# Optimization experiments

Measured on AMD Instinct MI355X. Metric: run time of the kernel, lower is better.

## Reference

```python
import jax, jax.numpy as jnp
import numpy as np

B, SM, SI, D, H, FF = 4, 1024, 4096, 256, 8, 1024
EPS = 1e-6

def _ln(x, g, b):
    m = jnp.mean(x, axis=-1, keepdims=True)
    v = jnp.mean(jnp.square(x - m), axis=-1, keepdims=True)
    return (x - m) * jax.lax.rsqrt(v + EPS) * g + b

def setup_inputs() -> dict:
    key = jax.random.key(0)
    ks = jax.random.split(key, 12)
    s = 0.02
    return {
        "state_seq": jax.random.normal(ks[0], (B, SM, D), jnp.float32),
        "input_seq": jax.random.normal(ks[1], (B, SI, D), jnp.float32),
        "Wk": jax.random.normal(ks[2], (D, D), jnp.float32) * s,
        "bk": jnp.zeros((D,), jnp.float32),
        "Wv": jax.random.normal(ks[3], (D, D), jnp.float32) * s,
        "bv": jnp.zeros((D,), jnp.float32),
        "Wq": jax.random.normal(ks[4], (H, D, D), jnp.float32) * s,
        "bq": jnp.zeros((H, D), jnp.float32),
        "Wo": jax.random.normal(ks[5], (H * D, D), jnp.float32) * s,
        "bo": jnp.zeros((D,), jnp.float32),
        "ln1_g": jnp.ones((D,), jnp.float32),
        "ln1_b": jnp.zeros((D,), jnp.float32),
        "W_in": jax.random.normal(ks[6], (D, FF), jnp.float32) * s,
        "b_in": jnp.zeros((FF,), jnp.float32),
        "Wg_nl": jax.random.normal(ks[7], (FF, FF), jnp.float32) * s,
        "bg_nl": jnp.zeros((FF,), jnp.float32),
        "Wg_l": jax.random.normal(ks[8], (FF, FF), jnp.float32) * s,
        "bg_l": jnp.zeros((FF,), jnp.float32),
        "Wg_o": jax.random.normal(ks[9], (FF, D), jnp.float32) * s,
        "bg_o": jnp.zeros((D,), jnp.float32),
        "ln2_g": jnp.ones((D,), jnp.float32),
        "ln2_b": jnp.zeros((D,), jnp.float32),
    }

def reference(state_seq, input_seq, Wk, bk, Wv, bv, Wq, bq, Wo, bo,
              ln1_g, ln1_b, W_in, b_in, Wg_nl, bg_nl, Wg_l, bg_l, Wg_o, bg_o,
              ln2_g, ln2_b):
    # shared key/value projections (multi-query: one K/V, many Q)
    ik = input_seq @ Wk + bk            # [B,SI,D]
    mk = state_seq @ Wk + bk            # [B,SM,D]
    iv = input_seq @ Wv + bv            # [B,SI,D]
    mv = state_seq @ Wv + bv            # [B,SM,D]
    # per-head queries from memory cells, stacked over H
    q = jnp.einsum('bmd,hde->hbme', state_seq, Wq) + bq[:, None, None, :]  # [H,B,SM,D]
    input_score = jnp.einsum('hbme,bse->hbms', q, ik)                      # [H,B,SM,SI]
    self_score = jnp.sum(q * mk[None], axis=-1, keepdims=True)             # [H,B,SM,1]
    score = jnp.concatenate([self_score, input_score], axis=-1)
    score = score / jnp.sqrt(jnp.asarray(D, score.dtype))
    attn = jax.nn.softmax(score, axis=-1)                                  # [H,B,SM,1+SI]
    val = jnp.einsum('hbms,bse->hbme', attn[..., 1:], iv) + attn[..., 0:1] * mv[None]
    concat = jnp.transpose(val, (1, 2, 0, 3)).reshape(val.shape[1], val.shape[2], -1)  # [B,SM,H*D]
    attn_out = concat @ Wo + bo
    x = _ln(attn_out + state_seq, ln1_g, ln1_b)
    h = jax.nn.relu(x @ W_in + b_in)                                       # [B,SM,FF]
    g = jax.nn.relu(h @ Wg_nl + bg_nl) * (h @ Wg_l + bg_l)
    ff = g @ Wg_o + bg_o
    return _ln(ff + x, ln2_g, ln2_b)
```

## Files before the change

### kernel.cpp

```cpp
#include <hip/hip_runtime.h>
#include <hip/hip_bf16.h>

typedef __bf16 bfx8 __attribute__((ext_vector_type(8)));
typedef __bf16 bfx4 __attribute__((ext_vector_type(4)));
typedef float  f32x4 __attribute__((ext_vector_type(4)));
typedef float  f32x16 __attribute__((ext_vector_type(16)));

#define MFMA16(a,b,c) __builtin_amdgcn_mfma_f32_16x16x32_bf16((a),(b),(c),0,0,0)
#define MFMA32(a,b,c) __builtin_amdgcn_mfma_f32_32x32x16_bf16((a),(b),(c),0,0,0)


#define PSCALE 0.09016844f
#define PCLAMP 43.2808512f

__device__ __forceinline__ unsigned cvtpk_bf16(float lo, float hi) {
  unsigned d;
  asm("v_cvt_pk_bf16_f32 %0, %1, %2" : "=v"(d) : "v"(lo), "v"(hi));
  return d;
}

__device__ __forceinline__ bfx8 packswap(const float* p) {
  unsigned a = cvtpk_bf16(p[0], p[1]);
  unsigned b = cvtpk_bf16(p[2], p[3]);
  unsigned c = cvtpk_bf16(p[4], p[5]);
  unsigned d = cvtpk_bf16(p[6], p[7]);
  asm("v_permlane32_swap_b32 %0, %1" : "+v"(a), "+v"(c));
  asm("v_permlane32_swap_b32 %0, %1" : "+v"(b), "+v"(d));
  union { unsigned u[4]; bfx8 v; } uu;
  uu.u[0] = a; uu.u[1] = b; uu.u[2] = c; uu.u[3] = d;
  return uu.v;
}

__device__ __forceinline__ void tile_tr(const float* __restrict__ src, __bf16* __restrict__ dst,
                                        int R, int C, int tile, float (*lt)[65]) {
  int tpr = C >> 6;
  int tr = tile / tpr, tc = tile % tpr;
  int c  = threadIdx.x & 63;
  int r0 = (threadIdx.x >> 6) << 4;
  const float* sp = src + (long)(tr * 64 + r0) * C + tc * 64 + c;
#pragma unroll
  for (int i = 0; i < 16; i++) lt[r0 + i][c] = sp[(long)i * C];
  __syncthreads();
  __bf16* dp = dst + (long)(tc * 64 + r0) * R + tr * 64 + c;
#pragma unroll
  for (int i = 0; i < 16; i++) dp[(long)i * R] = (__bf16)lt[c][r0 + i];
}

__global__ void trans_attn_t(const float* __restrict__ Wk, const float* __restrict__ Wv,
                             const float* __restrict__ Wq, const float* __restrict__ Wo,
                             __bf16* __restrict__ wkvqt, __bf16* __restrict__ wot) {
  __shared__ float lt[64][65];
  int t = blockIdx.x;
  if (t < 16)       tile_tr(Wk, wkvqt, 256, 256, t, lt);
  else if (t < 32)  tile_tr(Wv, wkvqt + 65536, 256, 256, t - 16, lt);
  else if (t < 160) {
    int e = t - 32, m = e >> 4;
    tile_tr(Wq + (long)m * 65536, wkvqt + 131072 + (long)m * 65536, 256, 256, e & 15, lt);
  } else            tile_tr(Wo, wot, 2048, 256, t - 160, lt);
}

__global__ void trans_ffn_t(const float* __restrict__ W_in, const float* __restrict__ Wg_nl,
                            const float* __restrict__ Wg_l, const float* __restrict__ Wg_o,
                            __bf16* __restrict__ dst) {
  __shared__ float lt[64][65];
  int t = blockIdx.x;
  if (t < 64)       tile_tr(W_in, dst, 256, 1024, t, lt);
  else if (t < 320) tile_tr(Wg_nl, dst + 262144, 1024, 1024, t - 64, lt);
  else if (t < 576) tile_tr(Wg_l, dst + 1310720, 1024, 1024, t - 320, lt);
  else              tile_tr(Wg_o, dst + 2359296, 1024, 256, t - 576, lt);
}

__device__ __forceinline__
void gemm_body(const __bf16* __restrict__ Xb, const float* __restrict__ Xf,
               const __bf16* __restrict__ Wt,
               const float* __restrict__ b1, const float* __restrict__ b2,
               const float* __restrict__ b3,
               __bf16* __restrict__ C, __bf16* __restrict__ C2, __bf16* __restrict__ C3,
               float* __restrict__ Cf,
               int M, int N, int Kfull, int kspan, int xmode, int mode, int act,
               int bx, int by, int bz, __bf16* xs, __bf16* wsm) {
  const int tid  = threadIdx.x;
  const int lane = tid & 63;
  const int w    = tid >> 6;
  const int l15  = lane & 15;
  const int quad = lane >> 4;
  const int wm   = (w >> 1) * 64;
  const int wn   = (w & 1) * 64;
  const int m0   = bx * 128;
  const int n0   = by * 128;
  const int k0   = (mode == 7) ? bz * kspan : 0;

  f32x4 acc[4][4];
#pragma unroll
  for (int i = 0; i < 4; i++)
#pragma unroll
    for (int j = 0; j < 4; j++) acc[i][j] = (f32x4){0.f, 0.f, 0.f, 0.f};

  for (int kk = k0; kk < k0 + kspan; kk += 64) {
    __syncthreads();
#pragma unroll
    for (int rep = 0; rep < 4; rep++) {
      int idx = rep * 256 + tid;
      int row = idx >> 3;
      int g   = idx & 7;
      if (xmode == 1) {
        const float* p = Xf + (long)(m0 + row) * Kfull + kk + g * 8;
        f32x4 a0 = *(const f32x4*)p;
        f32x4 a1 = *(const f32x4*)(p + 4);
        bfx8 v;
#pragma unroll
        for (int j = 0; j < 4; j++) { v[j] = (__bf16)a0[j]; v[4 + j] = (__bf16)a1[j]; }
        *(bfx8*)&xs[row * 72 + g * 8] = v;
      } else if (xmode == 2) {
        const __bf16* p = Xb + (long)(m0 + row) * 2048 + kk + g * 8;
        bfx8 a = *(const bfx8*)p;
        bfx8 bb = *(const bfx8*)(p + 1024);
        bfx8 v;
#pragma unroll
        for (int j = 0; j < 8; j++) v[j] = (__bf16)((float)a[j] * (float)bb[j]);
        *(bfx8*)&xs[row * 72 + g * 8] = v;
      } else {
        *(bfx8*)&xs[row * 72 + g * 8] = *(const bfx8*)(Xb + (long)(m0 + row) * Kfull + kk + g * 8);
      }
      *(bfx8*)&wsm[row * 72 + g * 8] = *(const bfx8*)(Wt + (long)(n0 + row) * Kfull + kk + g * 8);
    }
    __syncthreads();
#pragma unroll
    for (int ks = 0; ks < 2; ks++) {
      bfx8 af[4], bf_[4];
#pragma unroll
      for (int i = 0; i < 4; i++) af[i]  = *(const bfx8*)&xs[(wm + 16 * i + l15) * 72 + ks * 32 + quad * 8];
#pragma unroll
      for (int j = 0; j < 4; j++) bf_[j] = *(const bfx8*)&wsm[(wn + 16 * j + l15) * 72 + ks * 32 + quad * 8];
#pragma unroll
      for (int i = 0; i < 4; i++)
#pragma unroll
        for (int j = 0; j < 4; j++) acc[i][j] = MFMA16(af[i], bf_[j], acc[i][j]);
    }
  }

#pragma unroll
  for (int j = 0; j < 4; j++) {
    int n = n0 + wn + 16 * j + l15;
    float bv;
    if (mode == 4)      bv = (n < 256) ? b1[n] : b2[n - 256];
    else if (mode == 5) bv = (n < 256) ? b1[n] : (n < 512) ? b2[n - 256] : b3[n - 512];
    else if (mode == 6) bv = (n < 1024) ? b1[n] : b2[n - 1024];
    else if (mode == 7) bv = (bz == 0) ? b1[n] : 0.f;
    else                bv = b1[n];
#pragma unroll
    for (int i = 0; i < 4; i++) {
#pragma unroll
      for (int r = 0; r < 4; r++) {
        int m = m0 + wm + 16 * i + quad * 4 + r;
        float v = acc[i][j][r] + bv;
        if (mode == 6) { if (n < 1024) v = fmaxf(v, 0.f); }
        else if (act == 1) v = fmaxf(v, 0.f);
        if (mode == 4) {
          if (n < 256) C[(long)m * 256 + n] = (__bf16)v;
          else {
            int bb_ = m >> 12, si = m & 4095;
            C2[((long)(bb_ * 128 + (si >> 5)) * 256 + (n - 256)) * 32 + (si & 31)] = (__bf16)v;
          }
        } else if (mode == 5) {
          if (n < 256)      C[(long)m * 256 + n] = (__bf16)v;
          else if (n < 512) C2[(long)m * 256 + (n - 256)] = (__bf16)v;
          else {
            int nn = n - 512, hhh = nn >> 8, dd = nn & 255;
            C3[(long)hhh * 1048576 + (long)m * 256 + dd] = (__bf16)v;
          }
        } else if (mode == 7) {
          Cf[(long)bz * M * N + (long)m * N + n] = v;
        } else {
          C[(long)m * N + n] = (__bf16)v;
        }
      }
    }
  }
}

__global__ __launch_bounds__(256)
void gemm_bt(const __bf16* Xb, const float* Xf, const __bf16* Wt,
             const float* b1, const float* b2, const float* b3,
             __bf16* C, __bf16* C2, __bf16* C3, float* Cf,
             int M, int N, int Kfull, int kspan, int xmode, int mode, int act) {
  __shared__ __bf16 xs[128 * 72];
  __shared__ __bf16 wsm[128 * 72];
  gemm_body(Xb, Xf, Wt, b1, b2, b3, C, C2, C3, Cf, M, N, Kfull, kspan, xmode, mode, act,
            blockIdx.x, blockIdx.y, blockIdx.z, xs, wsm);
}

__global__ __launch_bounds__(256)
void proj2(const float* input, const float* state, const __bf16* Wkvqt,
           const float* bk, const float* bv, const float* bq,
           __bf16* ik, __bf16* ivT, __bf16* mk, __bf16* mv, __bf16* qbuf) {
  __shared__ __bf16 xs[128 * 72];
  __shared__ __bf16 wsm[128 * 72];
  int bid = blockIdx.x;
  if (bid < 512) {
    gemm_body(nullptr, input, Wkvqt, bk, bv, nullptr, ik, ivT, nullptr, nullptr,
              16384, 512, 256, 256, 1, 4, 0, bid & 127, bid >> 7, 0, xs, wsm);
  } else {
    int b2 = bid - 512;
    gemm_body(nullptr, state, Wkvqt, bk, bv, bq, mk, mv, qbuf, nullptr,
              4096, 2560, 256, 256, 1, 5, 0, b2 & 31, b2 >> 5, 0, xs, wsm);
  }
}

__global__ __attribute__((amdgpu_flat_work_group_size(512, 512)))
__attribute__((amdgpu_waves_per_eu(2, 2)))
void attn_kernel(const __bf16* __restrict__ qb,
                 const __bf16* __restrict__ ik,
                 const __bf16* __restrict__ ivT,
                 const __bf16* __restrict__ mk,
                 const __bf16* __restrict__ mv,
                 __bf16* __restrict__ concat) {
  __shared__ union {
    struct {
      __bf16 lk[2][2][32][264];
      __bf16 lvt[2][2][256][40];
    } s;
    float ex[4 * 8192 + 128];
  } sm;

  const int tid  = threadIdx.x;
  const int lane = tid & 63;
  const int w    = tid >> 6;
  const int half = w >> 2;
  const int wq   = w & 3;
  const int t256 = tid & 255;
  const int l31  = lane & 31;
  const int h    = lane >> 5;

  const int m0 = blockIdx.x * 128;
  const int b  = blockIdx.y;
  const int hh = blockIdx.z;
  const int mw = m0 + wq * 32;
  const int c0 = half * 64;

  const long qbase  = ((long)hh * 4096 + b * 1024 + mw) * 256;
  const long kvbase = (long)b * 4096 * 256;
  const long vtbase = (long)b * 128 * 8192;
  const long mbase  = ((long)b * 1024 + mw) * 256;

  bfx8 qf[16];
  {
    const __bf16* qrow = qb + qbase + (long)l31 * 256 + h * 8;
#pragma unroll
    for (int kt = 0; kt < 16; kt++) qf[kt] = *(const bfx8*)(qrow + kt * 16);
  }

  float ps_l;
  {
    const __bf16* krow = mk + mbase + (long)l31 * 256 + h * 8;
    float s = 0.f;
#pragma unroll
    for (int kt = 0; kt < 16; kt++) {
      bfx8 kv = *(const bfx8*)(krow + kt * 16);
#pragma unroll
      for (int j = 0; j < 8; j++) s += (float)qf[kt][j] * (float)kv[j];
    }
    s += __shfl_xor(s, 32);
    ps_l = __builtin_amdgcn_exp2f(fminf(s * PSCALE, PCLAMP));
  }

  f32x16 oacc[8];
#pragma unroll
  for (int dt = 0; dt < 8; dt++)
#pragma unroll
    for (int i = 0; i < 16; i++) oacc[dt][i] = 0.f;
  float den_l = 0.f;
  bfx8 pf0c, pf1c;

  f32x16 zz;
#pragma unroll
  for (int i = 0; i < 16; i++) zz[i] = 0.f;

  auto sload_k = [&](int c, bfx8* kreg) {
    const long kb = kvbase + (long)c * 8192;
#pragma unroll
    for (int rep = 0; rep < 4; rep++) {
      int idx = rep * 256 + t256;
      kreg[rep] = *(const bfx8*)(ik + kb + (long)(idx >> 5) * 256 + (idx & 31) * 8);
    }
  };
  auto sload_v = [&](int c, bfx8* vreg) {
    const long vb = vtbase + (long)c * 8192;
#pragma unroll
    for (int rep = 0; rep < 4; rep++) {
      int idx = rep * 256 + t256;
      vreg[rep] = *(const bfx8*)(ivT + vb + (long)idx * 8);
    }
  };
  auto sstore_k = [&](int slot, const bfx8* kreg) {
#pragma unroll
    for (int rep = 0; rep < 4; rep++) {
      int idx = rep * 256 + t256;
      *(bfx8*)&sm.s.lk[half][slot][idx >> 5][(idx & 31) * 8] = kreg[rep];
    }
  };
  auto sstore_v = [&](int slot, const bfx8* vreg) {
#pragma unroll
    for (int rep = 0; rep < 4; rep++) {
      int idx = rep * 256 + t256;
      *(bfx8*)&sm.s.lvt[half][slot][idx >> 2][(idx & 3) * 8] = vreg[rep];
    }
  };

  auto chunkMFMA = [&](int vslot, int kslot, bool doS, bool doPV, f32x16* sa) {
#pragma unroll
    for (int t = 0; t < 8; t++) {
      bfx8 vf0, vf1, kf0, kf1;
      if (doPV) {
        vf0 = *(const bfx8*)&sm.s.lvt[half][vslot][t * 32 + l31][h * 8];
        vf1 = *(const bfx8*)&sm.s.lvt[half][vslot][t * 32 + l31][16 + h * 8];
      }
      if (doS) {
        kf0 = *(const bfx8*)&sm.s.lk[half][kslot][l31][(2 * t) * 16 + h * 8];
        kf1 = *(const bfx8*)&sm.s.lk[half][kslot][l31][(2 * t + 1) * 16 + h * 8];
      }
      if (doPV) oacc[t] = MFMA32(pf0c, vf0, oacc[t]);
      if (doS) {
        if (t < 2) sa[2 * t] = MFMA32(kf0, qf[2 * t], zz);
        else       sa[(2 * t) & 3] = MFMA32(kf0, qf[2 * t], sa[(2 * t) & 3]);
      }
      if (doPV) oacc[t] = MFMA32(pf1c, vf1, oacc[t]);
      if (doS) {
        if (t < 2) sa[2 * t + 1] = MFMA32(kf1, qf[2 * t + 1], zz);
        else       sa[(2 * t + 1) & 3] = MFMA32(kf1, qf[2 * t + 1], sa[(2 * t + 1) & 3]);
      }
    }
  };

  auto finishP = [&](const f32x16* sa) {
    float p[16];
#pragma unroll
    for (int r = 0; r < 16; r++) {
      float s = (sa[0][r] + sa[1][r]) + (sa[2][r] + sa[3][r]);
      p[r] = __builtin_amdgcn_exp2f(fminf(s * PSCALE, PCLAMP));
      den_l += p[r];
    }
    pf0c = packswap(p);
    pf1c = packswap(p + 8);
  };

  {
    bfx8 kreg[4], vreg[4];
    sload_k(c0, kreg);
    sload_v(c0, vreg);
    sstore_k(0, kreg);
    sstore_v(0, vreg);
    sload_k(c0 + 1, kreg);
    sstore_k(1, kreg);
  }
  __syncthreads();

  f32x16 sa[4];
  chunkMFMA(0, 0, true, false, sa);
  finishP(sa);
  __syncthreads();

  for (int i = 0; i < 62; i++) {
    bfx8 kreg[4], vreg[4];
    sload_k(c0 + i + 2, kreg);
    sload_v(c0 + i + 1, vreg);
    chunkMFMA(i & 1, (i + 1) & 1, true, true, sa);
    sstore_k(i & 1, kreg);
    sstore_v((i + 1) & 1, vreg);
    finishP(sa);
    __syncthreads();
  }
  {
    bfx8 vreg[4];
    sload_v(c0 + 63, vreg);
    chunkMFMA(0, 1, true, true, sa);
    sstore_v(1, vreg);
    finishP(sa);
    __syncthreads();
  }
  chunkMFMA(1, 0, false, true, sa);
  __syncthreads();

  float den_row = den_l + __shfl_xor(den_l, 32);
  if (half == 1) {
    float* eo = sm.ex + wq * 8192;
#pragma unroll
    for (int dt = 0; dt < 8; dt++)
#pragma unroll
      for (int rq = 0; rq < 4; rq++) {
        f32x4 v4 = { oacc[dt][rq * 4 + 0], oacc[dt][rq * 4 + 1],
                     oacc[dt][rq * 4 + 2], oacc[dt][rq * 4 + 3] };
        *(f32x4*)&eo[(dt * 4 + rq) * 256 + lane * 4] = v4;
      }
    if (h == 0) sm.ex[4 * 8192 + wq * 32 + l31] = den_row;
  }
  __syncthreads();
  if (half == 0) {
    const float* eo = sm.ex + wq * 8192;
#pragma unroll
    for (int dt = 0; dt < 8; dt++)
#pragma unroll
      for (int rq = 0; rq < 4; rq++) {
        f32x4 v4 = *(const f32x4*)&eo[(dt * 4 + rq) * 256 + lane * 4];
#pragma unroll
        for (int j = 0; j < 4; j++) oacc[dt][rq * 4 + j] += v4[j];
      }
    float den1 = sm.ex[4 * 8192 + wq * 32 + l31];
    float tot  = den_row + den1 + ps_l;

#pragma unroll
    for (int r = 0; r < 16; r++) {
      int row = (r & 3) + 8 * (r >> 2) + 4 * h;
      float ps   = __shfl(ps_l, row);
      float dinv = 1.f / __shfl(tot, row);
      const __bf16* mvrow = mv + mbase + (long)row * 256;
      __bf16* crow = concat + ((long)(b * 1024 + mw + row)) * 2048 + hh * 256;
#pragma unroll
      for (int dt = 0; dt < 8; dt++) {
        int d = dt * 32 + l31;
        crow[d] = (__bf16)((oacc[dt][r] + ps * (float)mvrow[d]) * dinv);
      }
    }
  }
}

__global__ __launch_bounds__(256)
void attn_kernel_f(const __bf16* __restrict__ qb, const __bf16* __restrict__ ik,
                   const __bf16* __restrict__ ivT, const __bf16* __restrict__ mk,
                   const __bf16* __restrict__ mv, __bf16* __restrict__ concat) {
  __shared__ __bf16 lk[2][32][264];
  __shared__ __bf16 lvt[2][256][40];

  const int tid  = threadIdx.x;
  const int lane = tid & 63;
  const int w    = tid >> 6;
  const int l31  = lane & 31;
  const int h    = lane >> 5;

  const int m0 = blockIdx.x * 128;
  const int b  = blockIdx.y;
  const int hh = blockIdx.z;
  const int mw = m0 + w * 32;

  const long qbase  = ((long)hh * 4096 + b * 1024 + mw) * 256;
  const long kvbase = (long)b * 4096 * 256;
  const long vtbase = (long)b * 128 * 8192;
  const long mbase  = ((long)b * 1024 + mw) * 256;

  bfx8 qf[16];
  {
    const __bf16* qrow = qb + qbase + (long)l31 * 256 + h * 8;
#pragma unroll
    for (int kt = 0; kt < 16; kt++) qf[kt] = *(const bfx8*)(qrow + kt * 16);
  }

  float ps_l;
  {
    const __bf16* krow = mk + mbase + (long)l31 * 256 + h * 8;
    float s = 0.f;
#pragma unroll
    for (int kt = 0; kt < 16; kt++) {
      bfx8 kv = *(const bfx8*)(krow + kt * 16);
#pragma unroll
      for (int j = 0; j < 8; j++) s += (float)qf[kt][j] * (float)kv[j];
    }
    s += __shfl_xor(s, 32);
    ps_l = __builtin_amdgcn_exp2f(fminf(s * PSCALE, PCLAMP));
  }

  f32x16 oacc[8];
#pragma unroll
  for (int dt = 0; dt < 8; dt++)
#pragma unroll
    for (int i = 0; i < 16; i++) oacc[dt][i] = 0.f;
  float den_l = 0.f;
  bfx8 pf0c, pf1c;

  f32x16 zz;
#pragma unroll
  for (int i = 0; i < 16; i++) zz[i] = 0.f;

  auto sload_k = [&](int c, bfx8* kreg) {
    const long kb = kvbase + (long)c * 8192;
#pragma unroll
    for (int rep = 0; rep < 4; rep++) {
      int idx = rep * 256 + tid;
      kreg[rep] = *(const bfx8*)(ik + kb + (long)(idx >> 5) * 256 + (idx & 31) * 8);
    }
  };
  auto sload_v = [&](int c, bfx8* vreg) {
    const long vb = vtbase + (long)c * 8192;
#pragma unroll
    for (int rep = 0; rep < 4; rep++) {
      int idx = rep * 256 + tid;
      vreg[rep] = *(const bfx8*)(ivT + vb + (long)idx * 8);
    }
  };
  auto sstore_k = [&](int slot, const bfx8* kreg) {
#pragma unroll
    for (int rep = 0; rep < 4; rep++) {
      int idx = rep * 256 + tid;
      *(bfx8*)&lk[slot][idx >> 5][(idx & 31) * 8] = kreg[rep];
    }
  };
  auto sstore_v = [&](int slot, const bfx8* vreg) {
#pragma unroll
    for (int rep = 0; rep < 4; rep++) {
      int idx = rep * 256 + tid;
      *(bfx8*)&lvt[slot][idx >> 2][(idx & 3) * 8] = vreg[rep];
    }
  };

  auto chunkMFMA = [&](int vslot, int kslot, bool doS, bool doPV, f32x16* sa) {
#pragma unroll
    for (int t = 0; t < 8; t++) {
      bfx8 vf0, vf1, kf0, kf1;
      if (doPV) {
        vf0 = *(const bfx8*)&lvt[vslot][t * 32 + l31][h * 8];
        vf1 = *(const bfx8*)&lvt[vslot][t * 32 + l31][16 + h * 8];
      }
      if (doS) {
        kf0 = *(const bfx8*)&lk[kslot][l31][(2 * t) * 16 + h * 8];
        kf1 = *(const bfx8*)&lk[kslot][l31][(2 * t + 1) * 16 + h * 8];
      }
      if (doPV) oacc[t] = MFMA32(pf0c, vf0, oacc[t]);
      if (doS) {
        if (t < 2) sa[2 * t] = MFMA32(kf0, qf[2 * t], zz);
        else       sa[(2 * t) & 3] = MFMA32(kf0, qf[2 * t], sa[(2 * t) & 3]);
      }
      if (doPV) oacc[t] = MFMA32(pf1c, vf1, oacc[t]);
      if (doS) {
        if (t < 2) sa[2 * t + 1] = MFMA32(kf1, qf[2 * t + 1], zz);
        else       sa[(2 * t + 1) & 3] = MFMA32(kf1, qf[2 * t + 1], sa[(2 * t + 1) & 3]);
      }
    }
  };

  auto finishP = [&](const f32x16* sa) {
    float p[16];
#pragma unroll
    for (int r = 0; r < 16; r++) {
      float s = (sa[0][r] + sa[1][r]) + (sa[2][r] + sa[3][r]);
      p[r] = __builtin_amdgcn_exp2f(fminf(s * PSCALE, PCLAMP));
      den_l += p[r];
    }
    pf0c = packswap(p);
    pf1c = packswap(p + 8);
  };

  {
    bfx8 kreg[4], vreg[4];
    sload_k(0, kreg);
    sload_v(0, vreg);
    sstore_k(0, kreg);
    sstore_v(0, vreg);
    sload_k(1, kreg);
    sstore_k(1, kreg);
  }
  __syncthreads();

  f32x16 sa[4];
  chunkMFMA(0, 0, true, false, sa);
  finishP(sa);
  __syncthreads();

  for (int i = 0; i < 126; i++) {
    bfx8 kreg[4], vreg[4];
    sload_k(i + 2, kreg);
    sload_v(i + 1, vreg);
    chunkMFMA(i & 1, (i + 1) & 1, true, true, sa);
    sstore_k(i & 1, kreg);
    sstore_v((i + 1) & 1, vreg);
    finishP(sa);
    __syncthreads();
  }
  {
    bfx8 vreg[4];
    sload_v(127, vreg);
    chunkMFMA(0, 1, true, true, sa);
    sstore_v(1, vreg);
    finishP(sa);
    __syncthreads();
  }
  chunkMFMA(1, 0, false, true, sa);

  float tot = den_l + __shfl_xor(den_l, 32) + ps_l;
#pragma unroll
  for (int r = 0; r < 16; r++) {
    int row = (r & 3) + 8 * (r >> 2) + 4 * h;
    float ps   = __shfl(ps_l, row);
    float dinv = 1.f / __shfl(tot, row);
    const __bf16* mvrow = mv + mbase + (long)row * 256;
    __bf16* crow = concat + ((long)(b * 1024 + mw + row)) * 2048 + hh * 256;
#pragma unroll
    for (int dt = 0; dt < 8; dt++) {
      int d = dt * 32 + l31;
      crow[d] = (__bf16)((oacc[dt][r] + ps * (float)mvrow[d]) * dinv);
    }
  }
}

__global__ __launch_bounds__(256)
void ln4_kernel(const float* __restrict__ parts, const float* __restrict__ res,
                const float* __restrict__ g, const float* __restrict__ beta,
                __bf16* __restrict__ outb, float* __restrict__ outf) {
  int row  = blockIdx.x * 4 + (threadIdx.x >> 6);
  int lane = threadIdx.x & 63;
  const float* p = parts + (long)row * 256 + lane * 4;
  f32x4 a0 = *(const f32x4*)p;
  f32x4 a1 = *(const f32x4*)(p + 1048576);
  f32x4 a2 = *(const f32x4*)(p + 2097152);
  f32x4 a3 = *(const f32x4*)(p + 3145728);
  f32x4 rv = *(const f32x4*)(res + (long)row * 256 + lane * 4);
  float v[4], s1 = 0.f, s2 = 0.f;
#pragma unroll
  for (int i = 0; i < 4; i++) {
    v[i] = a0[i] + a1[i] + a2[i] + a3[i] + rv[i];
    s1 += v[i];
    s2 += v[i] * v[i];
  }
#pragma unroll
  for (int off = 32; off >= 1; off >>= 1) {
    s1 += __shfl_xor(s1, off);
    s2 += __shfl_xor(s2, off);
  }
  float mean = s1 * (1.f / 256.f);
  float var  = fmaxf(s2 * (1.f / 256.f) - mean * mean, 0.f);
  float rstd = rsqrtf(var + 1e-6f);
#pragma unroll
  for (int i = 0; i < 4; i++) {
    int c = lane * 4 + i;
    float o = (v[i] - mean) * rstd * g[c] + beta[c];
    if (outb) outb[(long)row * 256 + c] = (__bf16)o;
    if (outf) outf[(long)row * 256 + c] = o;
  }
}

extern "C" void kernel_launch(void* const* d_in, const int* in_sizes, int n_in,
                              void* d_out, int out_size, void* d_ws, size_t ws_size,
                              hipStream_t stream) {
  const float* state  = (const float*)d_in[0];
  const float* input  = (const float*)d_in[1];
  const float* Wk     = (const float*)d_in[2];
  const float* bk     = (const float*)d_in[3];
  const float* Wv     = (const float*)d_in[4];
  const float* bv     = (const float*)d_in[5];
  const float* Wq     = (const float*)d_in[6];
  const float* bq     = (const float*)d_in[7];
  const float* Wo     = (const float*)d_in[8];
  const float* bo     = (const float*)d_in[9];
  const float* ln1g   = (const float*)d_in[10];
  const float* ln1b   = (const float*)d_in[11];
  const float* W_in   = (const float*)d_in[12];
  const float* b_in   = (const float*)d_in[13];
  const float* Wg_nl  = (const float*)d_in[14];
  const float* bg_nl  = (const float*)d_in[15];
  const float* Wg_l   = (const float*)d_in[16];
  const float* bg_l   = (const float*)d_in[17];
  const float* Wg_o   = (const float*)d_in[18];
  const float* bg_o   = (const float*)d_in[19];
  const float* ln2g   = (const float*)d_in[20];
  const float* ln2b   = (const float*)d_in[21];
  float* out = (float*)d_out;

  const size_t needed_elems = 28442624;
  if (ws_size < needed_elems * sizeof(__bf16)) return;

  __bf16* ws = (__bf16*)d_ws;
  size_t off = 0;
  auto alloc = [&](size_t n) { __bf16* p = ws + off; off += n; return p; };
  __bf16* Wkvqt  = alloc(655360);
  __bf16* Wot    = alloc(524288);
  __bf16* ik     = alloc(4194304);
  __bf16* ivT    = alloc(4194304);
  __bf16* mk     = alloc(1048576);
  __bf16* mv     = alloc(1048576);
  __bf16* qbuf   = alloc(8388608);
  __bf16* concat = alloc(8388608);
  float*  wo_parts = (float*)qbuf;
  __bf16* x      = mv;
  __bf16* hbuf   = ik;
  __bf16* t12    = qbuf;
  float*  ff_parts = (float*)ik;
  __bf16* Wffn   = concat;
  float*  xf     = (float*)(concat + 3670016);

  static int use512 = -1;
  if (use512 < 0) {
    hipFuncAttributes fa{};
    hipError_t e = hipFuncGetAttributes(&fa, (const void*)attn_kernel);
    use512 = (e == hipSuccess && fa.localSizeBytes <= 16 && fa.numRegs >= 170) ? 1 : 0;
  }

  dim3 blk(256);

  trans_attn_t<<<dim3(288), blk, 0, stream>>>(Wk, Wv, Wq, Wo, Wkvqt, Wot);

  proj2<<<dim3(1152), blk, 0, stream>>>(input, state, Wkvqt, bk, bv, bq,
                                        ik, ivT, mk, mv, qbuf);

  if (use512)
    attn_kernel<<<dim3(8, 4, 8), dim3(512), 0, stream>>>(qbuf, ik, ivT, mk, mv, concat);
  else
    attn_kernel_f<<<dim3(8, 4, 8), blk, 0, stream>>>(qbuf, ik, ivT, mk, mv, concat);

  gemm_bt<<<dim3(32, 2, 4), blk, 0, stream>>>(concat, nullptr, Wot, bo, nullptr, nullptr,
                                              nullptr, nullptr, nullptr, wo_parts,
                                              4096, 256, 2048, 512, 0, 7, 0);
  ln4_kernel<<<dim3(1024), blk, 0, stream>>>(wo_parts, state, ln1g, ln1b, x, xf);

  trans_ffn_t<<<dim3(640), blk, 0, stream>>>(W_in, Wg_nl, Wg_l, Wg_o, Wffn);

  gemm_bt<<<dim3(32, 8), blk, 0, stream>>>(x, nullptr, Wffn, b_in, nullptr, nullptr,
                                           hbuf, nullptr, nullptr, nullptr,
                                           4096, 1024, 256, 256, 0, 0, 1);
  gemm_bt<<<dim3(32, 16), blk, 0, stream>>>(hbuf, nullptr, Wffn + 262144, bg_nl, bg_l, nullptr,
                                            t12, nullptr, nullptr, nullptr,
                                            4096, 2048, 1024, 1024, 0, 6, 0);
  gemm_bt<<<dim3(32, 2, 4), blk, 0, stream>>>(t12, nullptr, Wffn + 2359296, bg_o, nullptr, nullptr,
                                              nullptr, nullptr, nullptr, ff_parts,
                                              4096, 256, 1024, 256, 2, 7, 0);
  ln4_kernel<<<dim3(1024), blk, 0, stream>>>(ff_parts, xf, ln2g, ln2b, nullptr, out);
}
```

Before: 456.7 us.

## Split attention across output head-dim halves instead of key-sequence halves

Replaces the 512-thread attention kernel, which split the key sequence between two wave groups and merged partial outputs through shared memory, with a 256-thread kernel. The new kernel launches twice as many blocks, each owning half of the value/output dimension and iterating over all key chunks. This removes the LDS reduction and halves accumulator registers, which may allow higher occupancy. The cost is that every block recomputes the full QK^T scores and softmax, duplicating score MFMA work and K loads.

```diff
diff --git a/kernel.cpp b/kernel.cpp
--- a/kernel.cpp
+++ b/kernel.cpp
@@ -207,36 +207,27 @@
   }
 }
 
-__global__ __attribute__((amdgpu_flat_work_group_size(512, 512)))
-__attribute__((amdgpu_waves_per_eu(2, 2)))
-void attn_kernel(const __bf16* __restrict__ qb,
-                 const __bf16* __restrict__ ik,
-                 const __bf16* __restrict__ ivT,
-                 const __bf16* __restrict__ mk,
-                 const __bf16* __restrict__ mv,
-                 __bf16* __restrict__ concat) {
-  __shared__ union {
-    struct {
-      __bf16 lk[2][2][32][264];
-      __bf16 lvt[2][2][256][40];
-    } s;
-    float ex[4 * 8192 + 128];
-  } sm;
+__global__ __launch_bounds__(256)
+void attn_kernel_d(const __bf16* __restrict__ qb,
+                   const __bf16* __restrict__ ik,
+                   const __bf16* __restrict__ ivT,
+                   const __bf16* __restrict__ mk,
+                   const __bf16* __restrict__ mv,
+                   __bf16* __restrict__ concat) {
+  __shared__ __bf16 lk[2][32][264];
+  __shared__ __bf16 lvt[2][128][40];
 
   const int tid  = threadIdx.x;
   const int lane = tid & 63;
   const int w    = tid >> 6;
-  const int half = w >> 2;
-  const int wq   = w & 3;
-  const int t256 = tid & 255;
   const int l31  = lane & 31;
   const int h    = lane >> 5;
 
   const int m0 = blockIdx.x * 128;
   const int b  = blockIdx.y;
-  const int hh = blockIdx.z;
-  const int mw = m0 + wq * 32;
-  const int c0 = half * 64;
+  const int hh = blockIdx.z & 7;
+  const int dh = blockIdx.z >> 3;
+  const int mw = m0 + w * 32;
 
   const long qbase  = ((long)hh * 4096 + b * 1024 + mw) * 256;
   const long kvbase = (long)b * 4096 * 256;
@@ -264,9 +255,9 @@
     ps_l = __builtin_amdgcn_exp2f(fminf(s * PSCALE, PCLAMP));
   }
 
-  f32x16 oacc[8];
-#pragma unroll
-  for (int dt = 0; dt < 8; dt++)
+  f32x16 oacc[4];
+#pragma unroll
+  for (int dt = 0; dt < 4; dt++)
 #pragma unroll
     for (int i = 0; i < 16; i++) oacc[dt][i] = 0.f;
   float den_l = 0.f;
@@ -280,30 +271,30 @@
     const long kb = kvbase + (long)c * 8192;
 #pragma unroll
     for (int rep = 0; rep < 4; rep++) {
-      int idx = rep * 256 + t256;
+      int idx = rep * 256 + tid;
       kreg[rep] = *(const bfx8*)(ik + kb + (long)(idx >> 5) * 256 + (idx & 31) * 8);
     }
   };
   auto sload_v = [&](int c, bfx8* vreg) {
-    const long vb = vtbase + (long)c * 8192;
+    const long vb = vtbase + (long)c * 8192 + (long)dh * 4096;
+#pragma unroll
+    for (int rep = 0; rep < 2; rep++) {
+      int idx = rep * 256 + tid;
+      vreg[rep] = *(const bfx8*)(ivT + vb + (long)idx * 8);
+    }
+  };
+  auto sstore_k = [&](int slot, const bfx8* kreg) {
 #pragma unroll
     for (int rep = 0; rep < 4; rep++) {
-      int idx = rep * 256 + t256;
-      vreg[rep] = *(const bfx8*)(ivT + vb + (long)idx * 8);
-    }
-  };
-  auto sstore_k = [&](int slot, const bfx8* kreg) {
-#pragma unroll
-    for (int rep = 0; rep < 4; rep++) {
-      int idx = rep * 256 + t256;
-      *(bfx8*)&sm.s.lk[half][slot][idx >> 5][(idx & 31) * 8] = kreg[rep];
+      int idx = rep * 256 + tid;
+      *(bfx8*)&lk[slot][idx >> 5][(idx & 31) * 8] = kreg[rep];
     }
   };
   auto sstore_v = [&](int slot, const bfx8* vreg) {
 #pragma unroll
-    for (int rep = 0; rep < 4; rep++) {
-      int idx = rep * 256 + t256;
-      *(bfx8*)&sm.s.lvt[half][slot][idx >> 2][(idx & 3) * 8] = vreg[rep];
+    for (int rep = 0; rep < 2; rep++) {
+      int idx = rep * 256 + tid;
+      *(bfx8*)&lvt[slot][idx >> 2][(idx & 3) * 8] = vreg[rep];
     }
   };
 
@@ -311,20 +302,20 @@
 #pragma unroll
     for (int t = 0; t < 8; t++) {
       bfx8 vf0, vf1, kf0, kf1;
-      if (doPV) {
-        vf0 = *(const bfx8*)&sm.s.lvt[half][vslot][t * 32 + l31][h * 8];
-        vf1 = *(const bfx8*)&sm.s.lvt[half][vslot][t * 32 + l31][16 + h * 8];
+      if (doPV && t < 4) {
+        vf0 = *(const bfx8*)&lvt[vslot][t * 32 + l31][h * 8];
+        vf1 = *(const bfx8*)&lvt[vslot][t * 32 + l31][16 + h * 8];
       }
       if (doS) {
-        kf0 = *(const bfx8*)&sm.s.lk[half][kslot][l31][(2 * t) * 16 + h * 8];
-        kf1 = *(const bfx8*)&sm.s.lk[half][kslot][l31][(2 * t + 1) * 16 + h * 8];
-      }
-      if (doPV) oacc[t] = MFMA32(pf0c, vf0, oacc[t]);
+        kf0 = *(const bfx8*)&lk[kslot][l31][(2 * t) * 16 + h * 8];
+        kf1 = *(const bfx8*)&lk[kslot][l31][(2 * t + 1) * 16 + h * 8];
+      }
+      if (doPV && t < 4) oacc[t] = MFMA32(pf0c, vf0, oacc[t]);
       if (doS) {
         if (t < 2) sa[2 * t] = MFMA32(kf0, qf[2 * t], zz);
         else       sa[(2 * t) & 3] = MFMA32(kf0, qf[2 * t], sa[(2 * t) & 3]);
       }
-      if (doPV) oacc[t] = MFMA32(pf1c, vf1, oacc[t]);
+      if (doPV && t < 4) oacc[t] = MFMA32(pf1c, vf1, oacc[t]);
       if (doS) {
         if (t < 2) sa[2 * t + 1] = MFMA32(kf1, qf[2 * t + 1], zz);
         else       sa[(2 * t + 1) & 3] = MFMA32(kf1, qf[2 * t + 1], sa[(2 * t + 1) & 3]);
@@ -345,12 +336,12 @@
   };
 
   {
-    bfx8 kreg[4], vreg[4];
-    sload_k(c0, kreg);
-    sload_v(c0, vreg);
+    bfx8 kreg[4], vreg[2];
+    sload_k(0, kreg);
+    sload_v(0, vreg);
     sstore_k(0, kreg);
     sstore_v(0, vreg);
-    sload_k(c0 + 1, kreg);
+    sload_k(1, kreg);
     sstore_k(1, kreg);
   }
   __syncthreads();
@@ -360,10 +351,10 @@
   finishP(sa);
   __syncthreads();
 
-  for (int i = 0; i < 62; i++) {
-    bfx8 kreg[4], vreg[4];
-    sload_k(c0 + i + 2, kreg);
-    sload_v(c0 + i + 1, vreg);
+  for (int i = 0; i < 126; i++) {
+    bfx8 kreg[4], vreg[2];
+    sload_k(i + 2, kreg);
+    sload_v(i + 1, vreg);
     chunkMFMA(i & 1, (i + 1) & 1, true, true, sa);
     sstore_k(i & 1, kreg);
     sstore_v((i + 1) & 1, vreg);
@@ -371,55 +362,27 @@
     __syncthreads();
   }
   {
-    bfx8 vreg[4];
-    sload_v(c0 + 63, vreg);
+    bfx8 vreg[2];
+    sload_v(127, vreg);
     chunkMFMA(0, 1, true, true, sa);
     sstore_v(1, vreg);
     finishP(sa);
     __syncthreads();
   }
   chunkMFMA(1, 0, false, true, sa);
-  __syncthreads();
-
-  float den_row = den_l + __shfl_xor(den_l, 32);
-  if (half == 1) {
-    float* eo = sm.ex + wq * 8192;
-#pragma unroll
-    for (int dt = 0; dt < 8; dt++)
-#pragma unroll
-      for (int rq = 0; rq < 4; rq++) {
-        f32x4 v4 = { oacc[dt][rq * 4 + 0], oacc[dt][rq * 4 + 1],
-                     oacc[dt][rq * 4 + 2], oacc[dt][rq * 4 + 3] };
-        *(f32x4*)&eo[(dt * 4 + rq) * 256 + lane * 4] = v4;
-      }
-    if (h == 0) sm.ex[4 * 8192 + wq * 32 + l31] = den_row;
-  }
-  __syncthreads();
-  if (half == 0) {
-    const float* eo = sm.ex + wq * 8192;
-#pragma unroll
-    for (int dt = 0; dt < 8; dt++)
-#pragma unroll
-      for (int rq = 0; rq < 4; rq++) {
-        f32x4 v4 = *(const f32x4*)&eo[(dt * 4 + rq) * 256 + lane * 4];
-#pragma unroll
-        for (int j = 0; j < 4; j++) oacc[dt][rq * 4 + j] += v4[j];
-      }
-    float den1 = sm.ex[4 * 8192 + wq * 32 + l31];
-    float tot  = den_row + den1 + ps_l;
-
-#pragma unroll
-    for (int r = 0; r < 16; r++) {
-      int row = (r & 3) + 8 * (r >> 2) + 4 * h;
-      float ps   = __shfl(ps_l, row);
-      float dinv = 1.f / __shfl(tot, row);
-      const __bf16* mvrow = mv + mbase + (long)row * 256;
-      __bf16* crow = concat + ((long)(b * 1024 + mw + row)) * 2048 + hh * 256;
-#pragma unroll
-      for (int dt = 0; dt < 8; dt++) {
-        int d = dt * 32 + l31;
-        crow[d] = (__bf16)((oacc[dt][r] + ps * (float)mvrow[d]) * dinv);
-      }
+
+  float tot = den_l + __shfl_xor(den_l, 32) + ps_l;
+#pragma unroll
+  for (int r = 0; r < 16; r++) {
+    int row = (r & 3) + 8 * (r >> 2) + 4 * h;
+    float ps   = __shfl(ps_l, row);
+    float dinv = 1.f / __shfl(tot, row);
+    const __bf16* mvrow = mv + mbase + (long)row * 256 + dh * 128;
+    __bf16* crow = concat + ((long)(b * 1024 + mw + row)) * 2048 + hh * 256 + dh * 128;
+#pragma unroll
+    for (int dt = 0; dt < 4; dt++) {
+      int d = dt * 32 + l31;
+      crow[d] = (__bf16)((oacc[dt][r] + ps * (float)mvrow[d]) * dinv);
     }
   }
 }
@@ -685,11 +648,11 @@
   __bf16* Wffn   = concat;
   float*  xf     = (float*)(concat + 3670016);
 
-  static int use512 = -1;
-  if (use512 < 0) {
+  static int useD = -1;
+  if (useD < 0) {
     hipFuncAttributes fa{};
-    hipError_t e = hipFuncGetAttributes(&fa, (const void*)attn_kernel);
-    use512 = (e == hipSuccess && fa.localSizeBytes <= 16 && fa.numRegs >= 170) ? 1 : 0;
+    hipError_t e = hipFuncGetAttributes(&fa, (const void*)attn_kernel_d);
+    useD = (e == hipSuccess && fa.localSizeBytes <= 16) ? 1 : 0;
   }
 
   dim3 blk(256);
@@ -699,8 +662,8 @@
   proj2<<<dim3(1152), blk, 0, stream>>>(input, state, Wkvqt, bk, bv, bq,
                                         ik, ivT, mk, mv, qbuf);
 
-  if (use512)
-    attn_kernel<<<dim3(8, 4, 8), dim3(512), 0, stream>>>(qbuf, ik, ivT, mk, mv, concat);
+  if (useD)
+    attn_kernel_d<<<dim3(8, 4, 16), blk, 0, stream>>>(qbuf, ik, ivT, mk, mv, concat);
   else
     attn_kernel_f<<<dim3(8, 4, 8), blk, 0, stream>>>(qbuf, ik, ivT, mk, mv, concat);
 
```

Measured after the change: 547.0 us. 1.2x slower.
